# Kernel tuning notes

Measured on AMD Instinct MI355X. Metric: run time of the kernel, lower is better.

## Reference

```python
import jax, jax.numpy as jnp
import numpy as np

N_NODES = 50000
N_EDGES = 600000
N_GRAPHS = 100
IN_DIM, HID, OUT = 128, 128, 64
K = 2  # DGL TAGConv default hop count


def setup_inputs() -> dict:
    key = jax.random.key(0)
    ks = jax.random.split(key, 8)
    x = jax.random.normal(ks[0], (N_NODES, IN_DIM), dtype=jnp.float32)
    src = jax.random.randint(ks[1], (N_EDGES,), 0, N_NODES)
    dst = jax.random.randint(ks[2], (N_EDGES,), 0, N_NODES)
    graph_id = jnp.sort(jax.random.randint(ks[3], (N_NODES,), 0, N_GRAPHS))
    # TAGConv lin: Linear(in_feats*(K+1), out_feats), stored as (in*(K+1), out)
    W1 = jax.random.normal(ks[4], (IN_DIM * (K + 1), HID), dtype=jnp.float32) / np.sqrt(IN_DIM * (K + 1))
    b1 = jnp.zeros((HID,), dtype=jnp.float32)
    W2 = jax.random.normal(ks[5], (HID * (K + 1), OUT), dtype=jnp.float32) / np.sqrt(HID * (K + 1))
    b2 = jnp.zeros((OUT,), dtype=jnp.float32)
    return {"x": x, "W1": W1, "b1": b1, "W2": W2, "b2": b2,
            "src": src, "dst": dst, "graph_id": graph_id}


def _tagconv(h, src, dst, norm, W, b):
    """DGL TAGConv: relu(concat_k (D^-1/2 A D^-1/2)^k h @ W + b), k=0..K."""
    feats = [h]
    cur = h
    for _ in range(K):
        cur = cur * norm[:, None]
        cur = jax.ops.segment_sum(cur[src], dst, num_segments=N_NODES)
        cur = cur * norm[:, None]
        feats.append(cur)
    out = jnp.concatenate(feats, axis=-1) @ W + b
    return jax.nn.relu(out)


def reference(x, W1, b1, W2, b2, src, dst, graph_id):
    # symmetric norm from in-degrees (clamped to 1), as in DGL TAGConv
    deg = jax.ops.segment_sum(jnp.ones_like(dst, dtype=x.dtype), dst, num_segments=N_NODES)
    norm = jnp.clip(deg, 1.0, None) ** -0.5
    h = _tagconv(x, src, dst, norm, W1, b1)
    h = _tagconv(h, src, dst, norm, W2, b2)
    # MaxPooling readout: per-graph max over nodes
    return jax.ops.segment_max(h, graph_id, num_segments=N_GRAPHS)
```

## Files before the change

### kernel.cpp

```cpp
#include <hip/hip_runtime.h>
#include <hip/hip_bf16.h>

#define N_NODES 50000
#define N_EDGES 600000
#define N_GRAPHS 100
#define M_PAD 50176

typedef __bf16 bf16_t;
typedef __attribute__((ext_vector_type(8))) __bf16 bf16x8;
typedef __attribute__((ext_vector_type(2))) __bf16 bf16x2;
typedef __attribute__((ext_vector_type(4))) float f32x4;

__global__ void degk(const int* __restrict__ dst, int* __restrict__ deg, int n) {
    int i = blockIdx.x * 256 + threadIdx.x;
    if (i < n) atomicAdd(&deg[dst[i]], 1);
}

__global__ void normk(const int* __restrict__ deg, float* __restrict__ norm, int n) {
    int i = blockIdx.x * 256 + threadIdx.x;
    if (i < n) {
        float d = fmaxf((float)deg[i], 1.0f);
        norm[i] = 1.0f / sqrtf(d);
    }
}

__global__ __launch_bounds__(1024) void scan1(const int* __restrict__ deg,
                                              int* __restrict__ row_off,
                                              int* __restrict__ partial, int n) {
    __shared__ int buf[1024];
    int i = blockIdx.x * 1024 + threadIdx.x;
    int v = (i < n) ? deg[i] : 0;
    buf[threadIdx.x] = v;
    __syncthreads();
    for (int off = 1; off < 1024; off <<= 1) {
        int t = (threadIdx.x >= off) ? buf[threadIdx.x - off] : 0;
        __syncthreads();
        buf[threadIdx.x] += t;
        __syncthreads();
    }
    if (i < n) row_off[i + 1] = buf[threadIdx.x];
    if (threadIdx.x == 1023) partial[blockIdx.x] = buf[1023];
}

__global__ void scan2(int* __restrict__ partial, int nchunks) {
    int lane = threadIdx.x;
    int v = (lane < nchunks) ? partial[lane] : 0;
    for (int off = 1; off < 64; off <<= 1) {
        int t = __shfl_up(v, off, 64);
        if (lane >= off) v += t;
    }
    int ex = __shfl_up(v, 1, 64);
    if (lane == 0) ex = 0;
    if (lane < nchunks) partial[lane] = ex;
}

__global__ void scan3(int* __restrict__ row_off, const int* __restrict__ partial, int n) {
    int i = blockIdx.x * 256 + threadIdx.x;
    if (i == 0) row_off[0] = 0;
    if (i < n) row_off[i + 1] += partial[i >> 10];
}

__global__ void scatterk(const int* __restrict__ src, const int* __restrict__ dst,
                         const int* __restrict__ row_off, int* __restrict__ cursor,
                         int* __restrict__ csr_src, int n) {
    int e = blockIdx.x * 256 + threadIdx.x;
    if (e >= n) return;
    int d = dst[e];
    int pos = atomicAdd(&cursor[d], 1);
    csr_src[row_off[d] + pos] = src[e];
}

__global__ void prescale(const float* __restrict__ x, const float* __restrict__ norm,
                         bf16_t* __restrict__ xb, bf16_t* __restrict__ xs, int n) {
    int i = blockIdx.x * 256 + threadIdx.x;
    if (i >= n * 64) return;
    int node = i >> 6;
    int c = (i & 63) * 2;
    float2 v = *(const float2*)(x + (size_t)node * 128 + c);
    float nd = norm[node];
    bf16x2 vb; vb[0] = (bf16_t)v.x; vb[1] = (bf16_t)v.y;
    bf16x2 vs; vs[0] = (bf16_t)(v.x * nd); vs[1] = (bf16_t)(v.y * nd);
    *(bf16x2*)(xb + (size_t)node * 128 + c) = vb;
    *(bf16x2*)(xs + (size_t)node * 128 + c) = vs;
}

__global__ void permW(const float* __restrict__ W, bf16_t* __restrict__ Wp, int K, int N) {
    int i = blockIdx.x * 256 + threadIdx.x;
    if (i >= K * N) return;
    int k = i / N, n = i - k * N;
    int kt = k >> 5, q = (k >> 3) & 3, j = k & 7;
    int nt = n >> 4, ln = n & 15;
    int lane = q * 16 + ln;
    Wp[(((size_t)kt * (N >> 4) + nt) * 64 + lane) * 8 + j] = (bf16_t)W[i];
}

template <bool SCALED>
__global__ __launch_bounds__(256) void spmm_bf16(const bf16_t* __restrict__ in,
                                                 bf16_t* __restrict__ out_c,
                                                 bf16_t* __restrict__ out_s,
                                                 const float* __restrict__ norm,
                                                 const int* __restrict__ row_off,
                                                 const int* __restrict__ csr_src, int n) {
    int tid = threadIdx.x;
    int sub = tid >> 4;
    int l   = tid & 15;
    int node = blockIdx.x * 16 + sub;
    if (node >= n) return;
    int e0 = row_off[node], e1 = row_off[node + 1];
    const bf16_t* col = in + l * 8;
    float acc[8] = {};
    int e = e0;
    for (; e + 4 <= e1; e += 4) {
        int s0 = csr_src[e + 0];
        int s1 = csr_src[e + 1];
        int s2 = csr_src[e + 2];
        int s3 = csr_src[e + 3];
        bf16x8 v0 = *(const bf16x8*)(col + (size_t)s0 * 128);
        bf16x8 v1 = *(const bf16x8*)(col + (size_t)s1 * 128);
        bf16x8 v2 = *(const bf16x8*)(col + (size_t)s2 * 128);
        bf16x8 v3 = *(const bf16x8*)(col + (size_t)s3 * 128);
#pragma unroll
        for (int j = 0; j < 8; j++)
            acc[j] += ((float)v0[j] + (float)v1[j]) + ((float)v2[j] + (float)v3[j]);
    }
    for (; e < e1; e++) {
        int s = csr_src[e];
        bf16x8 v = *(const bf16x8*)(col + (size_t)s * 128);
#pragma unroll
        for (int j = 0; j < 8; j++) acc[j] += (float)v[j];
    }
    float nd = norm[node];
    bf16x8 oc, os;
#pragma unroll
    for (int j = 0; j < 8; j++) {
        float c = acc[j] * nd;
        oc[j] = (bf16_t)c;
        os[j] = (bf16_t)(c * nd);
    }
    *(bf16x8*)(out_c + (size_t)node * 128 + l * 8) = oc;
    if (SCALED) *(bf16x8*)(out_s + (size_t)node * 128 + l * 8) = os;
}

template <int NT, bool LAYER1>
__global__ __launch_bounds__(256) void gemm_mfma(const bf16_t* __restrict__ f0,
                                                 const bf16_t* __restrict__ f1,
                                                 const bf16_t* __restrict__ f2,
                                                 const bf16_t* __restrict__ Wp,
                                                 const float* __restrict__ bias,
                                                 const float* __restrict__ norm,
                                                 bf16_t* __restrict__ out_b,
                                                 bf16_t* __restrict__ out_s,
                                                 float* __restrict__ out_f, int M) {
    int wave = threadIdx.x >> 6;
    int lane = threadIdx.x & 63;
    int q = lane >> 4, ln = lane & 15;
    int row0 = blockIdx.x * 128 + wave * 32;

    f32x4 acc[2][NT] = {};
    const bf16_t* feats[3] = {f0, f1, f2};
    const bf16x8* Wf = (const bf16x8*)Wp;

#pragma unroll
    for (int kc = 0; kc < 12; kc++) {
        const bf16_t* A = feats[kc >> 2] + (size_t)(kc & 3) * 32 + q * 8;
        bf16x8 a0 = *(const bf16x8*)(A + (size_t)(row0 + ln) * 128);
        bf16x8 a1 = *(const bf16x8*)(A + (size_t)(row0 + 16 + ln) * 128);
        const bf16x8* Bp = Wf + (size_t)kc * NT * 64 + lane;
#pragma unroll
        for (int nt = 0; nt < NT; nt++) {
            bf16x8 b = Bp[nt * 64];
            acc[0][nt] = __builtin_amdgcn_mfma_f32_16x16x32_bf16(a0, b, acc[0][nt], 0, 0, 0);
            acc[1][nt] = __builtin_amdgcn_mfma_f32_16x16x32_bf16(a1, b, acc[1][nt], 0, 0, 0);
        }
    }

    float bv[NT];
#pragma unroll
    for (int nt = 0; nt < NT; nt++) bv[nt] = bias[nt * 16 + ln];

#pragma unroll
    for (int mt = 0; mt < 2; mt++) {
#pragma unroll
        for (int r = 0; r < 4; r++) {
            int row = row0 + mt * 16 + q * 4 + r;
            if (row >= M) continue;
            float nd = LAYER1 ? norm[row] : 0.f;
#pragma unroll
            for (int nt = 0; nt < NT; nt++) {
                int col = nt * 16 + ln;
                float val = fmaxf(acc[mt][nt][r] + bv[nt], 0.f);
                if (LAYER1) {
                    out_b[(size_t)row * 128 + col] = (bf16_t)val;
                    out_s[(size_t)row * 128 + col] = (bf16_t)(val * nd);
                } else {
                    out_f[(size_t)row * 64 + col] = val;
                }
            }
        }
    }
}

__global__ __launch_bounds__(256) void maxpool2(const float* __restrict__ hF,
                                                const int* __restrict__ gid,
                                                unsigned int* __restrict__ out, int n) {
    int wave = threadIdx.x >> 6;
    int lane = threadIdx.x & 63;
    int n0 = blockIdx.x * 256 + wave * 64;
    if (n0 >= n) return;
    int n1 = min(n0 + 64, n);
    int cur = gid[n0];
    float m = 0.f;
    int i = n0;
    for (; i + 4 <= n1; i += 4) {
        int g0 = gid[i + 0], g1 = gid[i + 1], g2 = gid[i + 2], g3 = gid[i + 3];
        float v0 = hF[(size_t)(i + 0) * 64 + lane];
        float v1 = hF[(size_t)(i + 1) * 64 + lane];
        float v2 = hF[(size_t)(i + 2) * 64 + lane];
        float v3 = hF[(size_t)(i + 3) * 64 + lane];
        if (g0 != cur) { atomicMax(&out[cur * 64 + lane], __float_as_uint(m)); cur = g0; m = v0; } else m = fmaxf(m, v0);
        if (g1 != cur) { atomicMax(&out[cur * 64 + lane], __float_as_uint(m)); cur = g1; m = v1; } else m = fmaxf(m, v1);
        if (g2 != cur) { atomicMax(&out[cur * 64 + lane], __float_as_uint(m)); cur = g2; m = v2; } else m = fmaxf(m, v2);
        if (g3 != cur) { atomicMax(&out[cur * 64 + lane], __float_as_uint(m)); cur = g3; m = v3; } else m = fmaxf(m, v3);
    }
    for (; i < n1; i++) {
        int g = gid[i];
        float v = hF[(size_t)i * 64 + lane];
        if (g != cur) { atomicMax(&out[cur * 64 + lane], __float_as_uint(m)); cur = g; m = v; }
        else m = fmaxf(m, v);
    }
    atomicMax(&out[cur * 64 + lane], __float_as_uint(m));
}

extern "C" void kernel_launch(void* const* d_in, const int* in_sizes, int n_in,
                              void* d_out, int out_size, void* d_ws, size_t ws_size,
                              hipStream_t stream) {
    const float* x  = (const float*)d_in[0];
    const float* W1 = (const float*)d_in[1];
    const float* b1 = (const float*)d_in[2];
    const float* W2 = (const float*)d_in[3];
    const float* b2 = (const float*)d_in[4];
    const int* src  = (const int*)d_in[5];
    const int* dst  = (const int*)d_in[6];
    const int* gid  = (const int*)d_in[7];
    float* out = (float*)d_out;

    char* ws = (char*)d_ws;
    size_t off = 0;
    auto take = [&](size_t bytes) {
        void* p = ws + off;
        off = (off + bytes + 255) & ~(size_t)255;
        return p;
    };
    int* deg     = (int*)take((size_t)N_NODES * 4);
    int* cursor  = (int*)take((size_t)N_NODES * 4);
    size_t zero_bytes = off;
    float* norm  = (float*)take((size_t)N_NODES * 4);
    int* row_off = (int*)take((size_t)(N_NODES + 1) * 4);
    int* partial = (int*)take(64 * 4);
    int* csr_src = (int*)take((size_t)N_EDGES * 4);
    bf16_t* Wp1  = (bf16_t*)take((size_t)384 * 128 * 2);
    bf16_t* Wp2  = (bf16_t*)take((size_t)384 * 64 * 2);
    bf16_t* B0 = (bf16_t*)take((size_t)M_PAD * 128 * 2);
    bf16_t* B1 = (bf16_t*)take((size_t)M_PAD * 128 * 2);
    bf16_t* B2 = (bf16_t*)take((size_t)M_PAD * 128 * 2);
    bf16_t* B3 = (bf16_t*)take((size_t)M_PAD * 128 * 2);
    bf16_t* B4 = (bf16_t*)take((size_t)M_PAD * 128 * 2);
    bf16_t* B5 = (bf16_t*)take((size_t)M_PAD * 128 * 2);
    (void)ws_size; (void)in_sizes; (void)n_in; (void)out_size;

    hipMemsetAsync(d_ws, 0, zero_bytes, stream);
    hipMemsetAsync(d_out, 0, (size_t)N_GRAPHS * 64 * 4, stream);

    degk<<<(N_EDGES + 255) / 256, 256, 0, stream>>>(dst, deg, N_EDGES);
    normk<<<(N_NODES + 255) / 256, 256, 0, stream>>>(deg, norm, N_NODES);

    int nchunks = (N_NODES + 1023) / 1024;
    scan1<<<nchunks, 1024, 0, stream>>>(deg, row_off, partial, N_NODES);
    scan2<<<1, 64, 0, stream>>>(partial, nchunks);
    scan3<<<(N_NODES + 255) / 256, 256, 0, stream>>>(row_off, partial, N_NODES);
    scatterk<<<(N_EDGES + 255) / 256, 256, 0, stream>>>(src, dst, row_off, cursor, csr_src, N_EDGES);

    prescale<<<(N_NODES * 64 + 255) / 256, 256, 0, stream>>>(x, norm, B0, B1, N_NODES);
    permW<<<(384 * 128 + 255) / 256, 256, 0, stream>>>(W1, Wp1, 384, 128);
    permW<<<(384 * 64 + 255) / 256, 256, 0, stream>>>(W2, Wp2, 384, 64);

    int spmm_grid = (N_NODES + 15) / 16;
    int gemm_grid = M_PAD / 128;
    spmm_bf16<true><<<spmm_grid, 256, 0, stream>>>(B1, B2, B4, norm, row_off, csr_src, N_NODES);
    spmm_bf16<false><<<spmm_grid, 256, 0, stream>>>(B4, B3, nullptr, norm, row_off, csr_src, N_NODES);
    gemm_mfma<8, true><<<gemm_grid, 256, 0, stream>>>(B0, B2, B3, Wp1, b1, norm, B5, B1, nullptr, N_NODES);
    spmm_bf16<true><<<spmm_grid, 256, 0, stream>>>(B1, B2, B4, norm, row_off, csr_src, N_NODES);
    spmm_bf16<false><<<spmm_grid, 256, 0, stream>>>(B4, B3, nullptr, norm, row_off, csr_src, N_NODES);
    gemm_mfma<4, false><<<gemm_grid, 256, 0, stream>>>(B5, B2, B3, Wp2, b2, nullptr, nullptr, nullptr, (float*)B0, N_NODES);
    maxpool2<<<(N_NODES + 255) / 256, 256, 0, stream>>>((const float*)B0, gid, (unsigned int*)out, N_NODES);
}
```

Measured before the change: 311.5 us.

## Column-tile SpMM into 32-wide slices and apply source norm on the fly

The SpMM is split into four 32-column tiles, so each block gathers only 64 bytes per neighbor row. The goal is to keep the gathered feature slice small enough to stay resident in cache. Source-side normalization is now applied inside the gather by reading norm[src], which removes the separately written scaled copies and two buffers. The norm kernel is folded into scan1 and the two weight-permute launches are merged into one. In exchange, every edge does an extra scalar norm load, each thread issues smaller 4-byte gathers, and the CSR index reads are repeated once per column tile.

```diff
diff --git a/kernel.cpp b/kernel.cpp
--- a/kernel.cpp
+++ b/kernel.cpp
@@ -8,6 +8,7 @@
 
 typedef __bf16 bf16_t;
 typedef __attribute__((ext_vector_type(8))) __bf16 bf16x8;
+typedef __attribute__((ext_vector_type(4))) __bf16 bf16x4;
 typedef __attribute__((ext_vector_type(2))) __bf16 bf16x2;
 typedef __attribute__((ext_vector_type(4))) float f32x4;
 
@@ -16,17 +17,10 @@
     if (i < n) atomicAdd(&deg[dst[i]], 1);
 }
 
-__global__ void normk(const int* __restrict__ deg, float* __restrict__ norm, int n) {
-    int i = blockIdx.x * 256 + threadIdx.x;
-    if (i < n) {
-        float d = fmaxf((float)deg[i], 1.0f);
-        norm[i] = 1.0f / sqrtf(d);
-    }
-}
-
 __global__ __launch_bounds__(1024) void scan1(const int* __restrict__ deg,
                                               int* __restrict__ row_off,
-                                              int* __restrict__ partial, int n) {
+                                              int* __restrict__ partial,
+                                              float* __restrict__ norm, int n) {
     __shared__ int buf[1024];
     int i = blockIdx.x * 1024 + threadIdx.x;
     int v = (i < n) ? deg[i] : 0;
@@ -38,7 +32,11 @@
         buf[threadIdx.x] += t;
         __syncthreads();
     }
-    if (i < n) row_off[i + 1] = buf[threadIdx.x];
+    if (i < n) {
+        row_off[i + 1] = buf[threadIdx.x];
+        float d = fmaxf((float)v, 1.0f);
+        norm[i] = 1.0f / sqrtf(d);
+    }
     if (threadIdx.x == 1023) partial[blockIdx.x] = buf[1023];
 }
 
@@ -70,75 +68,72 @@
     csr_src[row_off[d] + pos] = src[e];
 }
 
-__global__ void prescale(const float* __restrict__ x, const float* __restrict__ norm,
-                         bf16_t* __restrict__ xb, bf16_t* __restrict__ xs, int n) {
-    int i = blockIdx.x * 256 + threadIdx.x;
-    if (i >= n * 64) return;
-    int node = i >> 6;
-    int c = (i & 63) * 2;
-    float2 v = *(const float2*)(x + (size_t)node * 128 + c);
-    float nd = norm[node];
-    bf16x2 vb; vb[0] = (bf16_t)v.x; vb[1] = (bf16_t)v.y;
-    bf16x2 vs; vs[0] = (bf16_t)(v.x * nd); vs[1] = (bf16_t)(v.y * nd);
-    *(bf16x2*)(xb + (size_t)node * 128 + c) = vb;
-    *(bf16x2*)(xs + (size_t)node * 128 + c) = vs;
-}
-
-__global__ void permW(const float* __restrict__ W, bf16_t* __restrict__ Wp, int K, int N) {
-    int i = blockIdx.x * 256 + threadIdx.x;
-    if (i >= K * N) return;
-    int k = i / N, n = i - k * N;
+__global__ void prescale(const float* __restrict__ x, bf16_t* __restrict__ xb, int n) {
+    int i = blockIdx.x * 256 + threadIdx.x;
+    if (i >= n * 32) return;
+    float4 v = *(const float4*)(x + (size_t)i * 4);
+    bf16x4 o;
+    o[0] = (bf16_t)v.x; o[1] = (bf16_t)v.y; o[2] = (bf16_t)v.z; o[3] = (bf16_t)v.w;
+    *(bf16x4*)(xb + (size_t)i * 4) = o;
+}
+
+__global__ void permW2(const float* __restrict__ W1, bf16_t* __restrict__ Wp1,
+                       const float* __restrict__ W2, bf16_t* __restrict__ Wp2) {
+    int i = blockIdx.x * 256 + threadIdx.x;
+    const float* W; bf16_t* Wp; int N; int idx;
+    if (i < 384 * 128)            { W = W1; Wp = Wp1; N = 128; idx = i; }
+    else if (i < 384 * 128 + 384 * 64) { W = W2; Wp = Wp2; N = 64; idx = i - 384 * 128; }
+    else return;
+    int k = idx / N, n = idx - k * N;
     int kt = k >> 5, q = (k >> 3) & 3, j = k & 7;
     int nt = n >> 4, ln = n & 15;
     int lane = q * 16 + ln;
-    Wp[(((size_t)kt * (N >> 4) + nt) * 64 + lane) * 8 + j] = (bf16_t)W[i];
-}
-
-template <bool SCALED>
-__global__ __launch_bounds__(256) void spmm_bf16(const bf16_t* __restrict__ in,
-                                                 bf16_t* __restrict__ out_c,
-                                                 bf16_t* __restrict__ out_s,
-                                                 const float* __restrict__ norm,
-                                                 const int* __restrict__ row_off,
-                                                 const int* __restrict__ csr_src, int n) {
-    int tid = threadIdx.x;
-    int sub = tid >> 4;
-    int l   = tid & 15;
-    int node = blockIdx.x * 16 + sub;
+    Wp[(((size_t)kt * (N >> 4) + nt) * 64 + lane) * 8 + j] = (bf16_t)W[idx];
+}
+
+#define TILE_COLS 32
+__global__ __launch_bounds__(256) void spmm_t32(const bf16_t* __restrict__ in,
+                                                bf16_t* __restrict__ out,
+                                                const float* __restrict__ norm,
+                                                const int* __restrict__ row_off,
+                                                const int* __restrict__ csr_src,
+                                                int n, int nodeblocks) {
+    int tile = blockIdx.x / nodeblocks;
+    int nb   = blockIdx.x - tile * nodeblocks;
+    int tid  = threadIdx.x;
+    int sub  = tid >> 4;
+    int l    = tid & 15;
+    int node = nb * 16 + sub;
     if (node >= n) return;
     int e0 = row_off[node], e1 = row_off[node + 1];
-    const bf16_t* col = in + l * 8;
-    float acc[8] = {};
+    const bf16_t* colp = in + tile * TILE_COLS + l * 2;
+    float a0 = 0.f, a1 = 0.f;
     int e = e0;
     for (; e + 4 <= e1; e += 4) {
         int s0 = csr_src[e + 0];
         int s1 = csr_src[e + 1];
         int s2 = csr_src[e + 2];
         int s3 = csr_src[e + 3];
-        bf16x8 v0 = *(const bf16x8*)(col + (size_t)s0 * 128);
-        bf16x8 v1 = *(const bf16x8*)(col + (size_t)s1 * 128);
-        bf16x8 v2 = *(const bf16x8*)(col + (size_t)s2 * 128);
-        bf16x8 v3 = *(const bf16x8*)(col + (size_t)s3 * 128);
-#pragma unroll
-        for (int j = 0; j < 8; j++)
-            acc[j] += ((float)v0[j] + (float)v1[j]) + ((float)v2[j] + (float)v3[j]);
+        float n0 = norm[s0], n1 = norm[s1], n2 = norm[s2], n3 = norm[s3];
+        bf16x2 v0 = *(const bf16x2*)(colp + (size_t)s0 * 128);
+        bf16x2 v1 = *(const bf16x2*)(colp + (size_t)s1 * 128);
+        bf16x2 v2 = *(const bf16x2*)(colp + (size_t)s2 * 128);
+        bf16x2 v3 = *(const bf16x2*)(colp + (size_t)s3 * 128);
+        a0 += n0 * (float)v0[0] + n1 * (float)v1[0] + n2 * (float)v2[0] + n3 * (float)v3[0];
+        a1 += n0 * (float)v0[1] + n1 * (float)v1[1] + n2 * (float)v2[1] + n3 * (float)v3[1];
     }
     for (; e < e1; e++) {
         int s = csr_src[e];
-        bf16x8 v = *(const bf16x8*)(col + (size_t)s * 128);
-#pragma unroll
-        for (int j = 0; j < 8; j++) acc[j] += (float)v[j];
+        float ns = norm[s];
+        bf16x2 v = *(const bf16x2*)(colp + (size_t)s * 128);
+        a0 += ns * (float)v[0];
+        a1 += ns * (float)v[1];
     }
     float nd = norm[node];
-    bf16x8 oc, os;
-#pragma unroll
-    for (int j = 0; j < 8; j++) {
-        float c = acc[j] * nd;
-        oc[j] = (bf16_t)c;
-        os[j] = (bf16_t)(c * nd);
-    }
-    *(bf16x8*)(out_c + (size_t)node * 128 + l * 8) = oc;
-    if (SCALED) *(bf16x8*)(out_s + (size_t)node * 128 + l * 8) = os;
+    bf16x2 o;
+    o[0] = (bf16_t)(a0 * nd);
+    o[1] = (bf16_t)(a1 * nd);
+    __builtin_nontemporal_store(o, (bf16x2*)(out + (size_t)node * 128 + tile * TILE_COLS + l * 2));
 }
 
 template <int NT, bool LAYER1>
@@ -147,9 +142,7 @@
                                                  const bf16_t* __restrict__ f2,
                                                  const bf16_t* __restrict__ Wp,
                                                  const float* __restrict__ bias,
-                                                 const float* __restrict__ norm,
                                                  bf16_t* __restrict__ out_b,
-                                                 bf16_t* __restrict__ out_s,
                                                  float* __restrict__ out_f, int M) {
     int wave = threadIdx.x >> 6;
     int lane = threadIdx.x & 63;
@@ -184,14 +177,12 @@
         for (int r = 0; r < 4; r++) {
             int row = row0 + mt * 16 + q * 4 + r;
             if (row >= M) continue;
-            float nd = LAYER1 ? norm[row] : 0.f;
 #pragma unroll
             for (int nt = 0; nt < NT; nt++) {
                 int col = nt * 16 + ln;
                 float val = fmaxf(acc[mt][nt][r] + bv[nt], 0.f);
                 if (LAYER1) {
                     out_b[(size_t)row * 128 + col] = (bf16_t)val;
-                    out_s[(size_t)row * 128 + col] = (bf16_t)(val * nd);
                 } else {
                     out_f[(size_t)row * 64 + col] = val;
                 }
@@ -264,33 +255,30 @@
     bf16_t* B1 = (bf16_t*)take((size_t)M_PAD * 128 * 2);
     bf16_t* B2 = (bf16_t*)take((size_t)M_PAD * 128 * 2);
     bf16_t* B3 = (bf16_t*)take((size_t)M_PAD * 128 * 2);
-    bf16_t* B4 = (bf16_t*)take((size_t)M_PAD * 128 * 2);
-    bf16_t* B5 = (bf16_t*)take((size_t)M_PAD * 128 * 2);
     (void)ws_size; (void)in_sizes; (void)n_in; (void)out_size;
 
     hipMemsetAsync(d_ws, 0, zero_bytes, stream);
     hipMemsetAsync(d_out, 0, (size_t)N_GRAPHS * 64 * 4, stream);
 
+    prescale<<<(N_NODES * 32 + 255) / 256, 256, 0, stream>>>(x, B0, N_NODES);
+    permW2<<<(384 * 192 + 255) / 256, 256, 0, stream>>>(W1, Wp1, W2, Wp2);
+
     degk<<<(N_EDGES + 255) / 256, 256, 0, stream>>>(dst, deg, N_EDGES);
-    normk<<<(N_NODES + 255) / 256, 256, 0, stream>>>(deg, norm, N_NODES);
-
     int nchunks = (N_NODES + 1023) / 1024;
-    scan1<<<nchunks, 1024, 0, stream>>>(deg, row_off, partial, N_NODES);
+    scan1<<<nchunks, 1024, 0, stream>>>(deg, row_off, partial, norm, N_NODES);
     scan2<<<1, 64, 0, stream>>>(partial, nchunks);
     scan3<<<(N_NODES + 255) / 256, 256, 0, stream>>>(row_off, partial, N_NODES);
     scatterk<<<(N_EDGES + 255) / 256, 256, 0, stream>>>(src, dst, row_off, cursor, csr_src, N_EDGES);
 
-    prescale<<<(N_NODES * 64 + 255) / 256, 256, 0, stream>>>(x, norm, B0, B1, N_NODES);
-    permW<<<(384 * 128 + 255) / 256, 256, 0, stream>>>(W1, Wp1, 384, 128);
-    permW<<<(384 * 64 + 255) / 256, 256, 0, stream>>>(W2, Wp2, 384, 64);
-
-    int spmm_grid = (N_NODES + 15) / 16;
-    int gemm_grid = M_PAD / 128;
-    spmm_bf16<true><<<spmm_grid, 256, 0, stream>>>(B1, B2, B4, norm, row_off, csr_src, N_NODES);
-    spmm_bf16<false><<<spmm_grid, 256, 0, stream>>>(B4, B3, nullptr, norm, row_off, csr_src, N_NODES);
-    gemm_mfma<8, true><<<gemm_grid, 256, 0, stream>>>(B0, B2, B3, Wp1, b1, norm, B5, B1, nullptr, N_NODES);
-    spmm_bf16<true><<<spmm_grid, 256, 0, stream>>>(B1, B2, B4, norm, row_off, csr_src, N_NODES);
-    spmm_bf16<false><<<spmm_grid, 256, 0, stream>>>(B4, B3, nullptr, norm, row_off, csr_src, N_NODES);
-    gemm_mfma<4, false><<<gemm_grid, 256, 0, stream>>>(B5, B2, B3, Wp2, b2, nullptr, nullptr, nullptr, (float*)B0, N_NODES);
+    int nodeblocks = (N_NODES + 15) / 16;
+    int spmm_grid  = 4 * nodeblocks;
+    int gemm_grid  = M_PAD / 128;
+
+    spmm_t32<<<spmm_grid, 256, 0, stream>>>(B0, B1, norm, row_off, csr_src, N_NODES, nodeblocks);
+    spmm_t32<<<spmm_grid, 256, 0, stream>>>(B1, B2, norm, row_off, csr_src, N_NODES, nodeblocks);
+    gemm_mfma<8, true><<<gemm_grid, 256, 0, stream>>>(B0, B1, B2, Wp1, b1, B3, nullptr, N_NODES);
+    spmm_t32<<<spmm_grid, 256, 0, stream>>>(B3, B1, norm, row_off, csr_src, N_NODES, nodeblocks);
+    spmm_t32<<<spmm_grid, 256, 0, stream>>>(B1, B2, norm, row_off, csr_src, N_NODES, nodeblocks);
+    gemm_mfma<4, false><<<gemm_grid, 256, 0, stream>>>(B3, B1, B2, Wp2, b2, nullptr, (float*)B0, N_NODES);
     maxpool2<<<(N_NODES + 255) / 256, 256, 0, stream>>>((const float*)B0, gid, (unsigned int*)out, N_NODES);
 }
```

New measurement: 382.6 us. 1.23x slower.

## Fuse preprocessing kernels and unroll SpMM edge loop by eight

Applied to the files above, without the earlier changes.

Folds the norm computation into the first scan kernel. Replaces the separate partial-sum scan kernel with an in-block reduction inside scan3. Merges the prescale, CSR scatter and both weight permutations into one multi-role launch. The SpMM inner loop now gathers eight neighbours per iteration to raise memory-level parallelism. The aim is to cut launch overhead and idle gaps between small kernels, at the cost of more registers in the SpMM loop and block-divergent roles in the fused kernel.

```diff
diff --git a/kernel.cpp b/kernel.cpp
--- a/kernel.cpp
+++ b/kernel.cpp
@@ -8,6 +8,7 @@
 
 typedef __bf16 bf16_t;
 typedef __attribute__((ext_vector_type(8))) __bf16 bf16x8;
+typedef __attribute__((ext_vector_type(4))) __bf16 bf16x4;
 typedef __attribute__((ext_vector_type(2))) __bf16 bf16x2;
 typedef __attribute__((ext_vector_type(4))) float f32x4;
 
@@ -16,17 +17,10 @@
     if (i < n) atomicAdd(&deg[dst[i]], 1);
 }
 
-__global__ void normk(const int* __restrict__ deg, float* __restrict__ norm, int n) {
-    int i = blockIdx.x * 256 + threadIdx.x;
-    if (i < n) {
-        float d = fmaxf((float)deg[i], 1.0f);
-        norm[i] = 1.0f / sqrtf(d);
-    }
-}
-
 __global__ __launch_bounds__(1024) void scan1(const int* __restrict__ deg,
                                               int* __restrict__ row_off,
-                                              int* __restrict__ partial, int n) {
+                                              int* __restrict__ partial,
+                                              float* __restrict__ norm, int n) {
     __shared__ int buf[1024];
     int i = blockIdx.x * 1024 + threadIdx.x;
     int v = (i < n) ? deg[i] : 0;
@@ -38,60 +32,70 @@
         buf[threadIdx.x] += t;
         __syncthreads();
     }
-    if (i < n) row_off[i + 1] = buf[threadIdx.x];
+    if (i < n) {
+        row_off[i + 1] = buf[threadIdx.x];
+        float d = fmaxf((float)v, 1.0f);
+        norm[i] = 1.0f / sqrtf(d);
+    }
     if (threadIdx.x == 1023) partial[blockIdx.x] = buf[1023];
 }
 
-__global__ void scan2(int* __restrict__ partial, int nchunks) {
-    int lane = threadIdx.x;
-    int v = (lane < nchunks) ? partial[lane] : 0;
-    for (int off = 1; off < 64; off <<= 1) {
-        int t = __shfl_up(v, off, 64);
-        if (lane >= off) v += t;
-    }
-    int ex = __shfl_up(v, 1, 64);
-    if (lane == 0) ex = 0;
-    if (lane < nchunks) partial[lane] = ex;
-}
-
-__global__ void scan3(int* __restrict__ row_off, const int* __restrict__ partial, int n) {
+__global__ __launch_bounds__(256) void scan3(int* __restrict__ row_off,
+                                             const int* __restrict__ partial, int n) {
     int i = blockIdx.x * 256 + threadIdx.x;
+    int c = (blockIdx.x * 256) >> 10;
+    __shared__ int pre;
+    if (threadIdx.x < 64) {
+        int v = (threadIdx.x < c) ? partial[threadIdx.x] : 0;
+        for (int off = 32; off; off >>= 1) v += __shfl_down(v, off, 64);
+        if (threadIdx.x == 0) pre = v;
+    }
+    __syncthreads();
     if (i == 0) row_off[0] = 0;
-    if (i < n) row_off[i + 1] += partial[i >> 10];
-}
-
-__global__ void scatterk(const int* __restrict__ src, const int* __restrict__ dst,
-                         const int* __restrict__ row_off, int* __restrict__ cursor,
-                         int* __restrict__ csr_src, int n) {
-    int e = blockIdx.x * 256 + threadIdx.x;
-    if (e >= n) return;
-    int d = dst[e];
-    int pos = atomicAdd(&cursor[d], 1);
-    csr_src[row_off[d] + pos] = src[e];
-}
-
-__global__ void prescale(const float* __restrict__ x, const float* __restrict__ norm,
-                         bf16_t* __restrict__ xb, bf16_t* __restrict__ xs, int n) {
-    int i = blockIdx.x * 256 + threadIdx.x;
-    if (i >= n * 64) return;
-    int node = i >> 6;
-    int c = (i & 63) * 2;
-    float2 v = *(const float2*)(x + (size_t)node * 128 + c);
-    float nd = norm[node];
-    bf16x2 vb; vb[0] = (bf16_t)v.x; vb[1] = (bf16_t)v.y;
-    bf16x2 vs; vs[0] = (bf16_t)(v.x * nd); vs[1] = (bf16_t)(v.y * nd);
-    *(bf16x2*)(xb + (size_t)node * 128 + c) = vb;
-    *(bf16x2*)(xs + (size_t)node * 128 + c) = vs;
-}
-
-__global__ void permW(const float* __restrict__ W, bf16_t* __restrict__ Wp, int K, int N) {
-    int i = blockIdx.x * 256 + threadIdx.x;
-    if (i >= K * N) return;
-    int k = i / N, n = i - k * N;
-    int kt = k >> 5, q = (k >> 3) & 3, j = k & 7;
-    int nt = n >> 4, ln = n & 15;
-    int lane = q * 16 + ln;
-    Wp[(((size_t)kt * (N >> 4) + nt) * 64 + lane) * 8 + j] = (bf16_t)W[i];
+    if (i < n) row_off[i + 1] += pre;
+}
+
+#define NPRE 6250
+#define NSC  ((N_EDGES + 255) / 256)
+#define NPW  ((384 * 192 + 255) / 256)
+__global__ __launch_bounds__(256) void midk(const float* __restrict__ x,
+                                            const float* __restrict__ norm,
+                                            bf16_t* __restrict__ xb, bf16_t* __restrict__ xs,
+                                            const int* __restrict__ src, const int* __restrict__ dst,
+                                            const int* __restrict__ row_off, int* __restrict__ cursor,
+                                            int* __restrict__ csr_src,
+                                            const float* __restrict__ W1, bf16_t* __restrict__ Wp1,
+                                            const float* __restrict__ W2, bf16_t* __restrict__ Wp2) {
+    int b = blockIdx.x;
+    if (b < NPRE) {
+        int i = b * 256 + threadIdx.x;
+        int node = i >> 5, c4 = i & 31;
+        float4 v = *(const float4*)(x + (size_t)node * 128 + c4 * 4);
+        float nd = norm[node];
+        bf16x4 ob, os;
+        ob[0] = (bf16_t)v.x; ob[1] = (bf16_t)v.y; ob[2] = (bf16_t)v.z; ob[3] = (bf16_t)v.w;
+        os[0] = (bf16_t)(v.x * nd); os[1] = (bf16_t)(v.y * nd);
+        os[2] = (bf16_t)(v.z * nd); os[3] = (bf16_t)(v.w * nd);
+        *(bf16x4*)(xb + (size_t)node * 128 + c4 * 4) = ob;
+        *(bf16x4*)(xs + (size_t)node * 128 + c4 * 4) = os;
+    } else if (b < NPRE + NSC) {
+        int e = (b - NPRE) * 256 + threadIdx.x;
+        if (e >= N_EDGES) return;
+        int d = dst[e];
+        int pos = atomicAdd(&cursor[d], 1);
+        csr_src[row_off[d] + pos] = src[e];
+    } else {
+        int i = (b - NPRE - NSC) * 256 + threadIdx.x;
+        const float* W; bf16_t* Wp; int N; int idx;
+        if (i < 384 * 128)                 { W = W1; Wp = Wp1; N = 128; idx = i; }
+        else if (i < 384 * 128 + 384 * 64) { W = W2; Wp = Wp2; N = 64;  idx = i - 384 * 128; }
+        else return;
+        int k = idx / N, n = idx - k * N;
+        int kt = k >> 5, q = (k >> 3) & 3, j = k & 7;
+        int nt = n >> 4, ln = n & 15;
+        int lane = q * 16 + ln;
+        Wp[(((size_t)kt * (N >> 4) + nt) * 64 + lane) * 8 + j] = (bf16_t)W[idx];
+    }
 }
 
 template <bool SCALED>
@@ -110,7 +114,29 @@
     const bf16_t* col = in + l * 8;
     float acc[8] = {};
     int e = e0;
-    for (; e + 4 <= e1; e += 4) {
+    for (; e + 8 <= e1; e += 8) {
+        int s0 = csr_src[e + 0];
+        int s1 = csr_src[e + 1];
+        int s2 = csr_src[e + 2];
+        int s3 = csr_src[e + 3];
+        int s4 = csr_src[e + 4];
+        int s5 = csr_src[e + 5];
+        int s6 = csr_src[e + 6];
+        int s7 = csr_src[e + 7];
+        bf16x8 v0 = *(const bf16x8*)(col + (size_t)s0 * 128);
+        bf16x8 v1 = *(const bf16x8*)(col + (size_t)s1 * 128);
+        bf16x8 v2 = *(const bf16x8*)(col + (size_t)s2 * 128);
+        bf16x8 v3 = *(const bf16x8*)(col + (size_t)s3 * 128);
+        bf16x8 v4 = *(const bf16x8*)(col + (size_t)s4 * 128);
+        bf16x8 v5 = *(const bf16x8*)(col + (size_t)s5 * 128);
+        bf16x8 v6 = *(const bf16x8*)(col + (size_t)s6 * 128);
+        bf16x8 v7 = *(const bf16x8*)(col + (size_t)s7 * 128);
+#pragma unroll
+        for (int j = 0; j < 8; j++)
+            acc[j] += (((float)v0[j] + (float)v1[j]) + ((float)v2[j] + (float)v3[j]))
+                    + (((float)v4[j] + (float)v5[j]) + ((float)v6[j] + (float)v7[j]));
+    }
+    if (e + 4 <= e1) {
         int s0 = csr_src[e + 0];
         int s1 = csr_src[e + 1];
         int s2 = csr_src[e + 2];
@@ -122,6 +148,7 @@
 #pragma unroll
         for (int j = 0; j < 8; j++)
             acc[j] += ((float)v0[j] + (float)v1[j]) + ((float)v2[j] + (float)v3[j]);
+        e += 4;
     }
     for (; e < e1; e++) {
         int s = csr_src[e];
@@ -272,20 +299,15 @@
     hipMemsetAsync(d_out, 0, (size_t)N_GRAPHS * 64 * 4, stream);
 
     degk<<<(N_EDGES + 255) / 256, 256, 0, stream>>>(dst, deg, N_EDGES);
-    normk<<<(N_NODES + 255) / 256, 256, 0, stream>>>(deg, norm, N_NODES);
-
     int nchunks = (N_NODES + 1023) / 1024;
-    scan1<<<nchunks, 1024, 0, stream>>>(deg, row_off, partial, N_NODES);
-    scan2<<<1, 64, 0, stream>>>(partial, nchunks);
+    scan1<<<nchunks, 1024, 0, stream>>>(deg, row_off, partial, norm, N_NODES);
     scan3<<<(N_NODES + 255) / 256, 256, 0, stream>>>(row_off, partial, N_NODES);
-    scatterk<<<(N_EDGES + 255) / 256, 256, 0, stream>>>(src, dst, row_off, cursor, csr_src, N_EDGES);
-
-    prescale<<<(N_NODES * 64 + 255) / 256, 256, 0, stream>>>(x, norm, B0, B1, N_NODES);
-    permW<<<(384 * 128 + 255) / 256, 256, 0, stream>>>(W1, Wp1, 384, 128);
-    permW<<<(384 * 64 + 255) / 256, 256, 0, stream>>>(W2, Wp2, 384, 64);
+    midk<<<NPRE + NSC + NPW, 256, 0, stream>>>(x, norm, B0, B1, src, dst, row_off, cursor,
+                                               csr_src, W1, Wp1, W2, Wp2);
 
     int spmm_grid = (N_NODES + 15) / 16;
     int gemm_grid = M_PAD / 128;
+
     spmm_bf16<true><<<spmm_grid, 256, 0, stream>>>(B1, B2, B4, norm, row_off, csr_src, N_NODES);
     spmm_bf16<false><<<spmm_grid, 256, 0, stream>>>(B4, B3, nullptr, norm, row_off, csr_src, N_NODES);
     gemm_mfma<8, true><<<gemm_grid, 256, 0, stream>>>(B0, B2, B3, Wp1, b1, norm, B5, B1, nullptr, N_NODES);
```

New measurement: 310.2 us. No clear change (-0.4%).
